# Optimization experiments

Measured on AMD Instinct MI355X. Metric: run time of the kernel, lower is better.

The kernel has to match this reference:

```python
import jax, jax.numpy as jnp
import numpy as np

N = 100000   # nodes
E = 600000   # edges
DIN = 128
DOUT = 128
L = 4        # num_labels


def setup_inputs() -> dict:
    key = jax.random.key(0)
    ks = jax.random.split(key, 16)
    u = lambda k, s: jax.random.uniform(k, s, jnp.float32, -1.0, 1.0)
    return {
        "x": jax.random.normal(ks[0], (N, DIN), jnp.float32),
        "edge_index": jax.random.randint(ks[1], (2, E), 0, N, jnp.int32),
        "edge_label": jax.random.randint(ks[2], (E,), 0, L, jnp.int32),
        # self-loop linear (nn.Linear stored as [din, dout] for x @ W + b)
        "W_loop": u(ks[3], (DIN, DOUT)),
        "b_loop": u(ks[4], (DOUT,)),
        "W_loop_g": u(ks[5], (DIN, 1)),
        "b_loop_g": u(ks[6], (1,)),
        # conv_in (original edge direction)
        "W_in": u(ks[7], (DIN, DOUT)),
        "b_in": u(ks[8], (L, DOUT)),
        "W_in_g": u(ks[9], (DIN, 1)),
        "b_in_g": u(ks[10], (L, 1)),
        # conv_out (flipped edge direction)
        "W_out": u(ks[11], (DIN, DOUT)),
        "b_out": u(ks[12], (L, DOUT)),
        "W_out_g": u(ks[13], (DIN, 1)),
        "b_out_g": u(ks[14], (L, 1)),
    }


def _sgcn_dir(x, src, dst, lab, W, b_lab, W_g, b_lab_g):
    """Gather source node feats per edge, gated linear message, scatter-add to dst."""
    xj = x[src]                                        # [E, din]
    msg = xj @ W + b_lab[lab]                          # [E, dout]
    gate = jax.nn.sigmoid(xj @ W_g + b_lab_g[lab])     # [E, 1]
    return jax.ops.segment_sum(gate * msg, dst, num_segments=x.shape[0])


def reference(x, edge_index, edge_label,
              W_loop, b_loop, W_loop_g, b_loop_g,
              W_in, b_in, W_in_g, b_in_g,
              W_out, b_out, W_out_g, b_out_g):
    # self-loop: gated linear
    x_loop = jax.nn.sigmoid(x @ W_loop_g + b_loop_g) * (x @ W_loop + b_loop)
    src, dst = edge_index[0], edge_index[1]
    # PyG default flow: x_j = x[src], aggregate at dst
    x_in = _sgcn_dir(x, src, dst, edge_label, W_in, b_in, W_in_g, b_in_g)
    # flipped edge_index: x_j = x[dst], aggregate at src
    x_out = _sgcn_dir(x, dst, src, edge_label, W_out, b_out, W_out_g, b_out_g)
    return jax.nn.relu(x_loop + x_in + x_out)
```

## Files before the change

kernel.cpp:

```cpp
#include <hip/hip_runtime.h>
#include <math.h>

typedef float  f32x4  __attribute__((ext_vector_type(4)));
typedef short  bf16x8 __attribute__((ext_vector_type(8)));
typedef unsigned short u16x8 __attribute__((ext_vector_type(8)));

#define XROW 136

__device__ __forceinline__ float sigmoidf_(float v) {
    return 1.f / (1.f + __expf(-v));
}
__device__ __forceinline__ unsigned short f2b(float f) {
    union { float f; unsigned u; } c; c.f = f;
    const unsigned r = c.u + 0x7FFF + ((c.u >> 16) & 1);
    return (unsigned short)(r >> 16);
}
__device__ __forceinline__ float b2f(unsigned short u) {
    union { unsigned u; float f; } c; c.u = ((unsigned)u) << 16;
    return c.f;
}

__global__ __launch_bounds__(256) void conv_w(
    const float* __restrict__ Win, const float* __restrict__ Wout,
    const float* __restrict__ Wloop, unsigned short* __restrict__ Wt)
{
    const int t = blockIdx.x * 256 + threadIdx.x;
    if (t >= 3 * 16384) return;
    const int m = t >> 14;
    const int i = t & 16383;
    const int k = i >> 7, n = i & 127;
    const float* W = (m == 0) ? Win : ((m == 1) ? Wout : Wloop);
    Wt[m * 16384 + n * 128 + k] = f2b(W[i]);
}

__global__ __launch_bounds__(256) void sgcn_node_mfma(
    const float* __restrict__ x,
    const unsigned short* __restrict__ Wt,
    const float* __restrict__ b_loop,
    const float* __restrict__ W_loop_g, const float* __restrict__ b_loop_g,
    const float* __restrict__ W_in_g, const float* __restrict__ b_in_g,
    const float* __restrict__ W_out_g, const float* __restrict__ b_out_g,
    unsigned short* __restrict__ h_in, unsigned short* __restrict__ h_out,
    float* __restrict__ sg_in, float* __restrict__ sg_out,
    float* __restrict__ out, int N)
{
    __shared__ unsigned short xs[128 * XROW];
    __shared__ float gls[128];
    const int tid = threadIdx.x;
    const int n0 = blockIdx.x * 128;

    {
        const int row = tid >> 1;
        const int cb = (tid & 1) * 64;
        unsigned short* dst = &xs[row * XROW + cb];
        const int n = n0 + row;
        if (n < N) {
            const float* xr = x + (size_t)n * 128 + cb;
            #pragma unroll
            for (int i = 0; i < 64; i += 8) {
                const float4 v0 = *(const float4*)(xr + i);
                const float4 v1 = *(const float4*)(xr + i + 4);
                u16x8 pk;
                pk[0] = f2b(v0.x); pk[1] = f2b(v0.y); pk[2] = f2b(v0.z); pk[3] = f2b(v0.w);
                pk[4] = f2b(v1.x); pk[5] = f2b(v1.y); pk[6] = f2b(v1.z); pk[7] = f2b(v1.w);
                *(u16x8*)(dst + i) = pk;
            }
        } else {
            const u16x8 z = {0,0,0,0,0,0,0,0};
            #pragma unroll
            for (int i = 0; i < 64; i += 8) *(u16x8*)(dst + i) = z;
        }
    }
    __syncthreads();

    if (tid < 128) {
        const int n = n0 + tid;
        if (n < N) {
            float gl = 0.f, gi = 0.f, go = 0.f;
            const unsigned short* xr = &xs[tid * XROW];
            for (int kc = 0; kc < 128; kc += 8) {
                const u16x8 c = *(const u16x8*)(xr + kc);
                #pragma unroll
                for (int j = 0; j < 8; ++j) {
                    const float xv = b2f(c[j]);
                    gl = fmaf(xv, W_loop_g[kc + j], gl);
                    gi = fmaf(xv, W_in_g[kc + j], gi);
                    go = fmaf(xv, W_out_g[kc + j], go);
                }
            }
            gls[tid] = sigmoidf_(gl + b_loop_g[0]);
            #pragma unroll
            for (int l = 0; l < 4; ++l) {
                sg_in[(size_t)n * 4 + l]  = sigmoidf_(gi + b_in_g[l]);
                sg_out[(size_t)n * 4 + l] = sigmoidf_(go + b_out_g[l]);
            }
        } else {
            gls[tid] = 0.f;
        }
    }
    __syncthreads();

    const int w  = tid >> 6;
    const int l  = tid & 63;
    const int lr = l & 15;
    const int lk = l >> 4;
    const int rbase = w * 32;

    const unsigned short* a0p = &xs[(rbase + lr) * XROW + lk * 8];
    const unsigned short* a1p = &xs[(rbase + 16 + lr) * XROW + lk * 8];

    for (int ph = 0; ph < 3; ++ph) {
        const unsigned short* Wp = Wt + (size_t)ph * 16384;
        f32x4 acc[2][8];
        #pragma unroll
        for (int p = 0; p < 2; ++p)
            #pragma unroll
            for (int nt = 0; nt < 8; ++nt)
                acc[p][nt] = (f32x4){0.f, 0.f, 0.f, 0.f};

        #pragma unroll
        for (int ks = 0; ks < 4; ++ks) {
            const bf16x8 a0 = *(const bf16x8*)(a0p + ks * 32);
            const bf16x8 a1 = *(const bf16x8*)(a1p + ks * 32);
            #pragma unroll
            for (int nt = 0; nt < 8; ++nt) {
                const bf16x8 b = *(const bf16x8*)(Wp + (nt * 16 + lr) * 128 + ks * 32 + lk * 8);
                acc[0][nt] = __builtin_amdgcn_mfma_f32_16x16x32_bf16(a0, b, acc[0][nt], 0, 0, 0);
                acc[1][nt] = __builtin_amdgcn_mfma_f32_16x16x32_bf16(a1, b, acc[1][nt], 0, 0, 0);
            }
        }

        if (ph < 2) {
            unsigned short* hp = (ph == 0) ? h_in : h_out;
            #pragma unroll
            for (int p = 0; p < 2; ++p)
                #pragma unroll
                for (int r = 0; r < 4; ++r) {
                    const int node = n0 + rbase + p * 16 + lk * 4 + r;
                    if (node < N) {
                        unsigned short* row = hp + (size_t)node * 128 + lr;
                        #pragma unroll
                        for (int nt = 0; nt < 8; ++nt)
                            row[nt * 16] = f2b(acc[p][nt][r]);
                    }
                }
        } else {
            #pragma unroll
            for (int p = 0; p < 2; ++p)
                #pragma unroll
                for (int r = 0; r < 4; ++r) {
                    const int node = n0 + rbase + p * 16 + lk * 4 + r;
                    if (node < N) {
                        const float g = gls[rbase + p * 16 + lk * 4 + r];
                        float* row = out + (size_t)node * 128 + lr;
                        #pragma unroll
                        for (int nt = 0; nt < 8; ++nt)
                            row[nt * 16] = g * (acc[p][nt][r] + b_loop[nt * 16 + lr]);
                    }
                }
        }
    }
}

__global__ __launch_bounds__(256) void sgcn_zero(int* __restrict__ p, int n)
{
    const int i = blockIdx.x * blockDim.x + threadIdx.x;
    if (i < n) p[i] = 0;
}

__global__ __launch_bounds__(256) void sgcn_hist(
    const int* __restrict__ ei, int* __restrict__ cnt, int N, int E)
{
    const int e = blockIdx.x * blockDim.x + threadIdx.x;
    if (e < E) {
        atomicAdd(cnt + ei[E + e], 1);
        atomicAdd(cnt + N + ei[e], 1);
    }
}

__global__ __launch_bounds__(256) void scan_partial(
    const int* __restrict__ cnt, int* __restrict__ bsum, int M)
{
    const int t = threadIdx.x;
    const int base = blockIdx.x * 1024 + t * 4;
    int s = 0;
    if (base + 3 < M) {
        const int4 q = *(const int4*)(cnt + base);
        s = q.x + q.y + q.z + q.w;
    } else {
        for (int i = 0; i < 4; ++i) if (base + i < M) s += cnt[base + i];
    }
    #pragma unroll
    for (int off = 32; off; off >>= 1) s += __shfl_down(s, off, 64);
    __shared__ int red[4];
    if ((t & 63) == 0) red[t >> 6] = s;
    __syncthreads();
    if (t == 0) bsum[blockIdx.x] = red[0] + red[1] + red[2] + red[3];
}

__global__ __launch_bounds__(256) void scan_bsums(int* __restrict__ bsum, int B)
{
    __shared__ int part[256];
    const int t = threadIdx.x;
    const int K = (B + 255) / 256;
    const int lo = t * K;
    const int hi = min(lo + K, B);
    int s = 0;
    for (int i = lo; i < hi; ++i) s += bsum[i];
    part[t] = s;
    __syncthreads();
    for (int off = 1; off < 256; off <<= 1) {
        const int v = (t >= off) ? part[t - off] : 0;
        __syncthreads();
        part[t] += v;
        __syncthreads();
    }
    int run = (t > 0) ? part[t - 1] : 0;
    for (int i = lo; i < hi; ++i) {
        const int c = bsum[i];
        bsum[i] = run;
        run += c;
    }
}

__global__ __launch_bounds__(256) void scan_final(
    int* __restrict__ cnt, const int* __restrict__ bsum,
    int* __restrict__ row_in, int* __restrict__ row_out, int N, int E)
{
    const int t = threadIdx.x;
    const int base = blockIdx.x * 1024 + t * 4;
    const int M = 2 * N;
    int v0 = 0, v1 = 0, v2 = 0, v3 = 0;
    if (base + 3 < M) {
        const int4 q = *(const int4*)(cnt + base);
        v0 = q.x; v1 = q.y; v2 = q.z; v3 = q.w;
    } else {
        if (base     < M) v0 = cnt[base];
        if (base + 1 < M) v1 = cnt[base + 1];
        if (base + 2 < M) v2 = cnt[base + 2];
        if (base + 3 < M) v3 = cnt[base + 3];
    }
    const int s = v0 + v1 + v2 + v3;
    const int lane = t & 63;
    int inc = s;
    #pragma unroll
    for (int off = 1; off < 64; off <<= 1) {
        const int u = __shfl_up(inc, off, 64);
        if (lane >= off) inc += u;
    }
    __shared__ int wsum[4];
    if (lane == 63) wsum[t >> 6] = inc;
    __syncthreads();
    int wpre = 0;
    const int w = t >> 6;
    for (int i = 0; i < w; ++i) wpre += wsum[i];
    int run = bsum[blockIdx.x] + wpre + (inc - s);
    const int vv[4] = {v0, v1, v2, v3};
    #pragma unroll
    for (int i = 0; i < 4; ++i) {
        const int g = base + i;
        if (g < M) {
            if (g < N) row_in[g] = run; else row_out[g - N] = run;
            cnt[g] = run;
            run += vv[i];
        }
    }
    if (blockIdx.x == 0 && t == 0) { row_in[N] = E; row_out[N] = 2 * E; }
}

__global__ __launch_bounds__(256) void sgcn_fill(
    const int* __restrict__ ei, const int* __restrict__ lab,
    int* __restrict__ fill, int* __restrict__ idx, int N, int E)
{
    const int e = blockIdx.x * blockDim.x + threadIdx.x;
    if (e < E) {
        const int s = ei[e];
        const int d = ei[E + e];
        const int l = lab[e];
        const int pi = atomicAdd(fill + d, 1);
        idx[pi] = s * 4 + l;
        const int po = atomicAdd(fill + N + s, 1);
        idx[po] = d * 4 + l;
    }
}

__global__ __launch_bounds__(256) void sgcn_gather4(
    const unsigned short* __restrict__ h_in, const unsigned short* __restrict__ h_out,
    const float* __restrict__ sg_in, const float* __restrict__ sg_out,
    const int* __restrict__ row_in, const int* __restrict__ row_out,
    const int* __restrict__ idx,
    const float* __restrict__ b_in, const float* __restrict__ b_out,
    float* __restrict__ out, int N)
{
    const int lane = threadIdx.x & 63;
    const int node = (int)((blockIdx.x * (unsigned)blockDim.x + threadIdx.x) >> 6);
    if (node >= N) return;
    const int sub = lane >> 4;
    const int sl  = lane & 15;
    const int cb  = sl * 8;

    float acc[8];
    #pragma unroll
    for (int j = 0; j < 8; ++j) acc[j] = 0.f;
    float gi0 = 0.f, gi1 = 0.f, gi2 = 0.f, gi3 = 0.f;
    float go0 = 0.f, go1 = 0.f, go2 = 0.f, go3 = 0.f;

    {
        const int e1 = row_in[node + 1];
        for (int e = row_in[node] + sub; e < e1; e += 4) {
            const int p = idx[e];
            const float g = sg_in[p];
            const u16x8 hv = *(const u16x8*)(h_in + (size_t)(p >> 2) * 128 + cb);
            const int l = p & 3;
            gi0 += (l == 0) ? g : 0.f;
            gi1 += (l == 1) ? g : 0.f;
            gi2 += (l == 2) ? g : 0.f;
            gi3 += (l == 3) ? g : 0.f;
            #pragma unroll
            for (int j = 0; j < 8; ++j) acc[j] = fmaf(g, b2f(hv[j]), acc[j]);
        }
    }
    {
        const int e1 = row_out[node + 1];
        for (int e = row_out[node] + sub; e < e1; e += 4) {
            const int p = idx[e];
            const float g = sg_out[p];
            const u16x8 hv = *(const u16x8*)(h_out + (size_t)(p >> 2) * 128 + cb);
            const int l = p & 3;
            go0 += (l == 0) ? g : 0.f;
            go1 += (l == 1) ? g : 0.f;
            go2 += (l == 2) ? g : 0.f;
            go3 += (l == 3) ? g : 0.f;
            #pragma unroll
            for (int j = 0; j < 8; ++j) acc[j] = fmaf(g, b2f(hv[j]), acc[j]);
        }
    }

    #pragma unroll
    for (int j = 0; j < 8; ++j) {
        acc[j] += __shfl_xor(acc[j], 16, 64);
        acc[j] += __shfl_xor(acc[j], 32, 64);
    }
    gi0 += __shfl_xor(gi0, 16, 64); gi0 += __shfl_xor(gi0, 32, 64);
    gi1 += __shfl_xor(gi1, 16, 64); gi1 += __shfl_xor(gi1, 32, 64);
    gi2 += __shfl_xor(gi2, 16, 64); gi2 += __shfl_xor(gi2, 32, 64);
    gi3 += __shfl_xor(gi3, 16, 64); gi3 += __shfl_xor(gi3, 32, 64);
    go0 += __shfl_xor(go0, 16, 64); go0 += __shfl_xor(go0, 32, 64);
    go1 += __shfl_xor(go1, 16, 64); go1 += __shfl_xor(go1, 32, 64);
    go2 += __shfl_xor(go2, 16, 64); go2 += __shfl_xor(go2, 32, 64);
    go3 += __shfl_xor(go3, 16, 64); go3 += __shfl_xor(go3, 32, 64);

    if (sub == 0) {
        const float gis[4] = {gi0, gi1, gi2, gi3};
        const float gos[4] = {go0, go1, go2, go3};
        #pragma unroll
        for (int l = 0; l < 4; ++l) {
            const float4 bi0 = *(const float4*)(b_in + l * 128 + cb);
            const float4 bi1 = *(const float4*)(b_in + l * 128 + cb + 4);
            const float4 bo0 = *(const float4*)(b_out + l * 128 + cb);
            const float4 bo1 = *(const float4*)(b_out + l * 128 + cb + 4);
            acc[0] = fmaf(gis[l], bi0.x, fmaf(gos[l], bo0.x, acc[0]));
            acc[1] = fmaf(gis[l], bi0.y, fmaf(gos[l], bo0.y, acc[1]));
            acc[2] = fmaf(gis[l], bi0.z, fmaf(gos[l], bo0.z, acc[2]));
            acc[3] = fmaf(gis[l], bi0.w, fmaf(gos[l], bo0.w, acc[3]));
            acc[4] = fmaf(gis[l], bi1.x, fmaf(gos[l], bo1.x, acc[4]));
            acc[5] = fmaf(gis[l], bi1.y, fmaf(gos[l], bo1.y, acc[5]));
            acc[6] = fmaf(gis[l], bi1.z, fmaf(gos[l], bo1.z, acc[6]));
            acc[7] = fmaf(gis[l], bi1.w, fmaf(gos[l], bo1.w, acc[7]));
        }
        float* orow = out + (size_t)node * 128 + cb;
        float4 o0 = *(const float4*)orow;
        float4 o1 = *(const float4*)(orow + 4);
        o0.x = fmaxf(o0.x + acc[0], 0.f); o0.y = fmaxf(o0.y + acc[1], 0.f);
        o0.z = fmaxf(o0.z + acc[2], 0.f); o0.w = fmaxf(o0.w + acc[3], 0.f);
        o1.x = fmaxf(o1.x + acc[4], 0.f); o1.y = fmaxf(o1.y + acc[5], 0.f);
        o1.z = fmaxf(o1.z + acc[6], 0.f); o1.w = fmaxf(o1.w + acc[7], 0.f);
        *(float4*)orow = o0;
        *(float4*)(orow + 4) = o1;
    }
}

__global__ __launch_bounds__(256) void sgcn_scatter(
    const unsigned short* __restrict__ h_in, const unsigned short* __restrict__ h_out,
    const float* __restrict__ sg_in, const float* __restrict__ sg_out,
    const int* __restrict__ ei, const int* __restrict__ lab,
    const float* __restrict__ b_in, const float* __restrict__ b_out,
    float* __restrict__ out, int E)
{
    const int lane = threadIdx.x & 63;
    const int wid = (blockIdx.x * blockDim.x + threadIdx.x) >> 6;
    const int nw = (gridDim.x * blockDim.x) >> 6;
    const int c = lane * 2;

    for (int e = wid; e < E; e += nw) {
        const int s = ei[e];
        const int d = ei[E + e];
        const int l = lab[e];
        {
            const ushort2 hv = *(const ushort2*)(h_in + (size_t)s * 128 + c);
            const float2 bv = *(const float2*)(b_in + l * 128 + c);
            const float g = sg_in[(size_t)s * 4 + l];
            atomicAdd(out + (size_t)d * 128 + c,     g * (b2f(hv.x) + bv.x));
            atomicAdd(out + (size_t)d * 128 + c + 1, g * (b2f(hv.y) + bv.y));
        }
        {
            const ushort2 hv = *(const ushort2*)(h_out + (size_t)d * 128 + c);
            const float2 bv = *(const float2*)(b_out + l * 128 + c);
            const float g = sg_out[(size_t)d * 4 + l];
            atomicAdd(out + (size_t)s * 128 + c,     g * (b2f(hv.x) + bv.x));
            atomicAdd(out + (size_t)s * 128 + c + 1, g * (b2f(hv.y) + bv.y));
        }
    }
}

__global__ __launch_bounds__(256) void sgcn_relu(float* __restrict__ out, long total4)
{
    const long i = (long)blockIdx.x * blockDim.x + threadIdx.x;
    if (i < total4) {
        float4 v = ((float4*)out)[i];
        v.x = fmaxf(v.x, 0.f); v.y = fmaxf(v.y, 0.f);
        v.z = fmaxf(v.z, 0.f); v.w = fmaxf(v.w, 0.f);
        ((float4*)out)[i] = v;
    }
}

extern "C" void kernel_launch(void* const* d_in, const int* in_sizes, int n_in,
                              void* d_out, int out_size, void* d_ws, size_t ws_size,
                              hipStream_t stream)
{
    const float* x        = (const float*)d_in[0];
    const int*   ei       = (const int*)d_in[1];
    const int*   lab      = (const int*)d_in[2];
    const float* W_loop   = (const float*)d_in[3];
    const float* b_loop   = (const float*)d_in[4];
    const float* W_loop_g = (const float*)d_in[5];
    const float* b_loop_g = (const float*)d_in[6];
    const float* W_in     = (const float*)d_in[7];
    const float* b_in     = (const float*)d_in[8];
    const float* W_in_g   = (const float*)d_in[9];
    const float* b_in_g   = (const float*)d_in[10];
    const float* W_out    = (const float*)d_in[11];
    const float* b_out    = (const float*)d_in[12];
    const float* W_out_g  = (const float*)d_in[13];
    const float* b_out_g  = (const float*)d_in[14];

    const int N = in_sizes[0] / 128;
    const int E = in_sizes[1] / 2;
    const int M = 2 * N;
    const int B = (M + 1023) / 1024;

    unsigned short* h_in  = (unsigned short*)d_ws;
    unsigned short* h_out = h_in + (size_t)N * 128;
    float* sg_in  = (float*)(h_out + (size_t)N * 128);
    float* sg_out = sg_in + (size_t)N * 4;
    unsigned short* Wt = (unsigned short*)(sg_out + (size_t)N * 4);
    int* row_in  = (int*)(Wt + 3 * 16384);
    int* row_out = row_in + (N + 1);
    int* cnt     = row_out + (N + 1);
    int* bsum    = cnt + M;
    int* idx     = bsum + ((B + 3) & ~3);
    const size_t need = ((size_t)(idx + 2 * (size_t)E) - (size_t)d_ws);

    float* out = (float*)d_out;
    dim3 blk(256);

    conv_w<<<dim3(192), blk, 0, stream>>>(W_in, W_out, W_loop, Wt);

    sgcn_node_mfma<<<dim3((N + 127) / 128), blk, 0, stream>>>(
        x, Wt, b_loop, W_loop_g, b_loop_g, W_in_g, b_in_g, W_out_g, b_out_g,
        h_in, h_out, sg_in, sg_out, out, N);

    if (need <= ws_size) {
        sgcn_zero<<<dim3((M + 255) / 256), blk, 0, stream>>>(cnt, M);
        sgcn_hist<<<dim3((E + 255) / 256), blk, 0, stream>>>(ei, cnt, N, E);
        scan_partial<<<dim3(B), blk, 0, stream>>>(cnt, bsum, M);
        scan_bsums<<<dim3(1), blk, 0, stream>>>(bsum, B);
        scan_final<<<dim3(B), blk, 0, stream>>>(cnt, bsum, row_in, row_out, N, E);
        sgcn_fill<<<dim3((E + 255) / 256), blk, 0, stream>>>(ei, lab, cnt, idx, N, E);
        sgcn_gather4<<<dim3((N * 64 + 255) / 256), blk, 0, stream>>>(
            h_in, h_out, sg_in, sg_out, row_in, row_out, idx, b_in, b_out, out, N);
    } else {
        sgcn_scatter<<<dim3(2048), blk, 0, stream>>>(
            h_in, h_out, sg_in, sg_out, ei, lab, b_in, b_out, out, E);
        const long total4 = (long)N * 128 / 4;
        sgcn_relu<<<dim3((unsigned)((total4 + 255) / 256)), blk, 0, stream>>>(out, total4);
    }
}
```

Baseline: 322.4 us.

## Fuse weight conversion with histogram and pack gate values into CSR entries

Merges the weight bf16 transpose kernel and the edge-degree histogram into one launch, and replaces the zeroing kernel with hipMemsetAsync. The fill kernel now looks up each edge's gate value and stores it next to the neighbor index as an int2, so the gather kernel no longer does a dependent random read of sg_in/sg_out. The aim is fewer launches and a shorter dependent-load chain in the gather loop. The cost is twice the index memory and extra random reads during fill.

Measured after the change: 300.1 us. 1.07x faster.

```diff
diff --git a/kernel.cpp b/kernel.cpp
--- a/kernel.cpp
+++ b/kernel.cpp
@@ -20,17 +20,26 @@
     return c.f;
 }
 
-__global__ __launch_bounds__(256) void conv_w(
+__global__ __launch_bounds__(256) void prep_hist(
     const float* __restrict__ Win, const float* __restrict__ Wout,
-    const float* __restrict__ Wloop, unsigned short* __restrict__ Wt)
-{
-    const int t = blockIdx.x * 256 + threadIdx.x;
-    if (t >= 3 * 16384) return;
-    const int m = t >> 14;
-    const int i = t & 16383;
-    const int k = i >> 7, n = i & 127;
-    const float* W = (m == 0) ? Win : ((m == 1) ? Wout : Wloop);
-    Wt[m * 16384 + n * 128 + k] = f2b(W[i]);
+    const float* __restrict__ Wloop, unsigned short* __restrict__ Wt,
+    const int* __restrict__ ei, int* __restrict__ cnt, int N, int E_hist, int E)
+{
+    if (blockIdx.x < 192) {
+        const int t = blockIdx.x * 256 + threadIdx.x;
+        if (t >= 3 * 16384) return;
+        const int m = t >> 14;
+        const int i = t & 16383;
+        const int k = i >> 7, n = i & 127;
+        const float* W = (m == 0) ? Win : ((m == 1) ? Wout : Wloop);
+        Wt[m * 16384 + n * 128 + k] = f2b(W[i]);
+    } else {
+        const int e = (blockIdx.x - 192) * 256 + threadIdx.x;
+        if (e < E_hist) {
+            atomicAdd(cnt + ei[E + e], 1);
+            atomicAdd(cnt + N + ei[e], 1);
+        }
+    }
 }
 
 __global__ __launch_bounds__(256) void sgcn_node_mfma(
@@ -162,22 +171,6 @@
     }
 }
 
-__global__ __launch_bounds__(256) void sgcn_zero(int* __restrict__ p, int n)
-{
-    const int i = blockIdx.x * blockDim.x + threadIdx.x;
-    if (i < n) p[i] = 0;
-}
-
-__global__ __launch_bounds__(256) void sgcn_hist(
-    const int* __restrict__ ei, int* __restrict__ cnt, int N, int E)
-{
-    const int e = blockIdx.x * blockDim.x + threadIdx.x;
-    if (e < E) {
-        atomicAdd(cnt + ei[E + e], 1);
-        atomicAdd(cnt + N + ei[e], 1);
-    }
-}
-
 __global__ __launch_bounds__(256) void scan_partial(
     const int* __restrict__ cnt, int* __restrict__ bsum, int M)
 {
@@ -270,7 +263,8 @@
 
 __global__ __launch_bounds__(256) void sgcn_fill(
     const int* __restrict__ ei, const int* __restrict__ lab,
-    int* __restrict__ fill, int* __restrict__ idx, int N, int E)
+    const float* __restrict__ sg_in, const float* __restrict__ sg_out,
+    int* __restrict__ fill, int2* __restrict__ idx2, int N, int E)
 {
     const int e = blockIdx.x * blockDim.x + threadIdx.x;
     if (e < E) {
@@ -278,17 +272,16 @@
         const int d = ei[E + e];
         const int l = lab[e];
         const int pi = atomicAdd(fill + d, 1);
-        idx[pi] = s * 4 + l;
+        idx2[pi] = make_int2(s * 4 + l, __float_as_int(sg_in[(size_t)s * 4 + l]));
         const int po = atomicAdd(fill + N + s, 1);
-        idx[po] = d * 4 + l;
-    }
-}
-
-__global__ __launch_bounds__(256) void sgcn_gather4(
+        idx2[po] = make_int2(d * 4 + l, __float_as_int(sg_out[(size_t)d * 4 + l]));
+    }
+}
+
+__global__ __launch_bounds__(256) void sgcn_gather4g(
     const unsigned short* __restrict__ h_in, const unsigned short* __restrict__ h_out,
-    const float* __restrict__ sg_in, const float* __restrict__ sg_out,
     const int* __restrict__ row_in, const int* __restrict__ row_out,
-    const int* __restrict__ idx,
+    const int2* __restrict__ idx2,
     const float* __restrict__ b_in, const float* __restrict__ b_out,
     float* __restrict__ out, int N)
 {
@@ -308,10 +301,10 @@
     {
         const int e1 = row_in[node + 1];
         for (int e = row_in[node] + sub; e < e1; e += 4) {
-            const int p = idx[e];
-            const float g = sg_in[p];
-            const u16x8 hv = *(const u16x8*)(h_in + (size_t)(p >> 2) * 128 + cb);
-            const int l = p & 3;
+            const int2 pq = idx2[e];
+            const float g = __int_as_float(pq.y);
+            const u16x8 hv = *(const u16x8*)(h_in + (size_t)(pq.x >> 2) * 128 + cb);
+            const int l = pq.x & 3;
             gi0 += (l == 0) ? g : 0.f;
             gi1 += (l == 1) ? g : 0.f;
             gi2 += (l == 2) ? g : 0.f;
@@ -323,10 +316,10 @@
     {
         const int e1 = row_out[node + 1];
         for (int e = row_out[node] + sub; e < e1; e += 4) {
-            const int p = idx[e];
-            const float g = sg_out[p];
-            const u16x8 hv = *(const u16x8*)(h_out + (size_t)(p >> 2) * 128 + cb);
-            const int l = p & 3;
+            const int2 pq = idx2[e];
+            const float g = __int_as_float(pq.y);
+            const u16x8 hv = *(const u16x8*)(h_out + (size_t)(pq.x >> 2) * 128 + cb);
+            const int l = pq.x & 3;
             go0 += (l == 0) ? g : 0.f;
             go1 += (l == 1) ? g : 0.f;
             go2 += (l == 2) ? g : 0.f;
@@ -458,27 +451,32 @@
     int* row_out = row_in + (N + 1);
     int* cnt     = row_out + (N + 1);
     int* bsum    = cnt + M;
-    int* idx     = bsum + ((B + 3) & ~3);
-    const size_t need = ((size_t)(idx + 2 * (size_t)E) - (size_t)d_ws);
+    int2* idx2   = (int2*)(((size_t)(bsum + B) + 15) & ~(size_t)15);
+    const size_t need = ((size_t)(idx2 + 2 * (size_t)E) - (size_t)d_ws);
 
     float* out = (float*)d_out;
     dim3 blk(256);
-
-    conv_w<<<dim3(192), blk, 0, stream>>>(W_in, W_out, W_loop, Wt);
+    const bool csr = (need <= ws_size);
+
+    if (csr) hipMemsetAsync(cnt, 0, (size_t)M * sizeof(int), stream);
+
+    const int E_hist = csr ? E : 0;
+    const int hist_blocks = csr ? (E + 255) / 256 : 0;
+    prep_hist<<<dim3(192 + hist_blocks), blk, 0, stream>>>(
+        W_in, W_out, W_loop, Wt, ei, cnt, N, E_hist, E);
 
     sgcn_node_mfma<<<dim3((N + 127) / 128), blk, 0, stream>>>(
         x, Wt, b_loop, W_loop_g, b_loop_g, W_in_g, b_in_g, W_out_g, b_out_g,
         h_in, h_out, sg_in, sg_out, out, N);
 
-    if (need <= ws_size) {
-        sgcn_zero<<<dim3((M + 255) / 256), blk, 0, stream>>>(cnt, M);
-        sgcn_hist<<<dim3((E + 255) / 256), blk, 0, stream>>>(ei, cnt, N, E);
+    if (csr) {
         scan_partial<<<dim3(B), blk, 0, stream>>>(cnt, bsum, M);
         scan_bsums<<<dim3(1), blk, 0, stream>>>(bsum, B);
         scan_final<<<dim3(B), blk, 0, stream>>>(cnt, bsum, row_in, row_out, N, E);
-        sgcn_fill<<<dim3((E + 255) / 256), blk, 0, stream>>>(ei, lab, cnt, idx, N, E);
-        sgcn_gather4<<<dim3((N * 64 + 255) / 256), blk, 0, stream>>>(
-            h_in, h_out, sg_in, sg_out, row_in, row_out, idx, b_in, b_out, out, N);
+        sgcn_fill<<<dim3((E + 255) / 256), blk, 0, stream>>>(
+            ei, lab, sg_in, sg_out, cnt, idx2, N, E);
+        sgcn_gather4g<<<dim3((N * 64 + 255) / 256), blk, 0, stream>>>(
+            h_in, h_out, row_in, row_out, idx2, b_in, b_out, out, N);
     } else {
         sgcn_scatter<<<dim3(2048), blk, 0, stream>>>(
             h_in, h_out, sg_in, sg_out, ei, lab, b_in, b_out, out, E);
```
